# Kernel optimization log

Hardware: AMD Instinct MI355X
Metric: run time of the kernel (lower is better)

Reference implementation:

```python
import jax, jax.numpy as jnp
import numpy as np

V, P, H, NH, D, L, FF, W, NCLS = 50265, 4098, 768, 12, 64, 12, 3072, 256, 43

def _ln(x, g, b):
    m = jnp.mean(x, -1, keepdims=True)
    v = jnp.mean((x - m) ** 2, -1, keepdims=True)
    return (x - m) * jax.lax.rsqrt(v + 1e-5) * g + b

def _sliding_attn(h, mask, wq, bq, wk, bk, wv, bv):
    # Longformer sliding-window attention, one-sided window W=256 (total 513).
    B, S, _ = h.shape
    C = S // W  # number of query chunks
    split = lambda x: x.reshape(B, S, NH, D).transpose(0, 2, 1, 3)  # [B,NH,S,D]
    q = split(h @ wq + bq) * (1.0 / np.sqrt(D))
    k = split(h @ wk + bk)
    v = split(h @ wv + bv)
    # keys/values needed by query chunk c span absolute positions [c*W - W, c*W + 2W)
    idx = jnp.arange(3 * W)[None, :] + W * jnp.arange(C)[:, None]  # [C,3W] into padded seq
    kb = jnp.pad(k, ((0, 0), (0, 0), (W, W), (0, 0)))[:, :, idx]  # [B,NH,C,3W,D]
    vb = jnp.pad(v, ((0, 0), (0, 0), (W, W), (0, 0)))[:, :, idx]
    qc = q.reshape(B, NH, C, W, D)
    s = jnp.einsum('bhcqd,bhckd->bhcqk', qc, kb)  # [B,NH,C,W,3W]
    r = jnp.arange(W)[:, None]
    t = jnp.arange(3 * W)[None, :]
    band = (t - r >= 0) & (t - r <= 2 * W)  # |key_pos - query_pos| <= W
    km = jnp.pad(mask, ((0, 0), (W, W)))[:, idx] > 0  # [B,C,3W] valid (non-pad) keys
    m = band[None, None, None] & km[:, None, :, None, :]  # [B,1,C,W,3W]
    p = jax.nn.softmax(jnp.where(m, s, -1e9), axis=-1)
    o = jnp.einsum('bhcqk,bhckd->bhcqd', p, vb).reshape(B, NH, S, D)
    return o.transpose(0, 2, 1, 3).reshape(B, S, NH * D)

def _forward(input_ids, attention_mask, word_emb, pos_emb, tok_emb, emb_ln_g, emb_ln_b,
             Wq, bq, Wk, bk, Wv, bv, Wo, bo, ln1_g, ln1_b, Wi, bi, Wo2, bo2, ln2_g, ln2_b,
             cls_w1, cls_b1, cls_w2, cls_b2):
    B, S = input_ids.shape
    pos = jnp.arange(S) + 2  # RoBERTa-style offset (padding_idx=1)
    h = word_emb[input_ids] + pos_emb[pos][None] + tok_emb[0][None, None]
    h = _ln(h, emb_ln_g, emb_ln_b)
    mask = attention_mask
    def block(h, p):
        wq, bq_, wk, bk_, wv, bv_, wo, bo_, g1, b1, wi, bi_, wo2, bo2_, g2, b2 = p
        a = _sliding_attn(h, mask, wq, bq_, wk, bk_, wv, bv_)
        h = _ln(h + a @ wo + bo_, g1, b1)
        f = jax.nn.gelu(h @ wi + bi_, approximate=False)
        h = _ln(h + f @ wo2 + bo2_, g2, b2)
        return h, None
    h, _ = jax.lax.scan(block, h, (Wq, bq, Wk, bk, Wv, bv, Wo, bo, ln1_g, ln1_b,
                                   Wi, bi, Wo2, bo2, ln2_g, ln2_b))
    pooled = h[:, 0]  # CLS token
    x = jax.nn.relu(pooled @ cls_w1 + cls_b1)
    return x @ cls_w2 + cls_b2

def setup_inputs() -> dict:
    key = jax.random.key(0)
    ks = iter(jax.random.split(key, 64))
    def rn(shape):
        return jax.random.normal(next(ks), shape, dtype=jnp.float32) * 0.02
    return {
        'input_ids': jax.random.randint(next(ks), (2, 4096), 0, V, dtype=jnp.int32),
        'attention_mask': jnp.ones((2, 4096), dtype=jnp.int32),
        'word_emb': rn((V, H)), 'pos_emb': rn((P, H)), 'tok_emb': rn((1, H)),
        'emb_ln_g': jnp.ones(H), 'emb_ln_b': jnp.zeros(H),
        'Wq': rn((L, H, H)), 'bq': jnp.zeros((L, H)),
        'Wk': rn((L, H, H)), 'bk': jnp.zeros((L, H)),
        'Wv': rn((L, H, H)), 'bv': jnp.zeros((L, H)),
        'Wo': rn((L, H, H)), 'bo': jnp.zeros((L, H)),
        'ln1_g': jnp.ones((L, H)), 'ln1_b': jnp.zeros((L, H)),
        'Wi': rn((L, H, FF)), 'bi': jnp.zeros((L, FF)),
        'Wo2': rn((L, FF, H)), 'bo2': jnp.zeros((L, H)),
        'ln2_g': jnp.ones((L, H)), 'ln2_b': jnp.zeros((L, H)),
        'cls_w1': rn((H, 512)), 'cls_b1': jnp.zeros(512),
        'cls_w2': rn((512, NCLS)), 'cls_b2': jnp.zeros(NCLS),
    }

def reference(input_ids, attention_mask, word_emb, pos_emb, tok_emb, emb_ln_g, emb_ln_b,
              Wq, bq, Wk, bk, Wv, bv, Wo, bo, ln1_g, ln1_b, Wi, bi, Wo2, bo2, ln2_g, ln2_b,
              cls_w1, cls_b1, cls_w2, cls_b2):
    return _forward(input_ids, attention_mask, word_emb, pos_emb, tok_emb, emb_ln_g, emb_ln_b,
                    Wq, bq, Wk, bk, Wv, bv, Wo, bo, ln1_g, ln1_b, Wi, bi, Wo2, bo2, ln2_g, ln2_b,
                    cls_w1, cls_b1, cls_w2, cls_b2)
```

## Files before the change

### kernel.cpp

```cpp
#include <hip/hip_runtime.h>
#include <hip/hip_bf16.h>

typedef unsigned short u16;
typedef __attribute__((ext_vector_type(8))) short short8;
typedef __attribute__((ext_vector_type(4))) float f32x4;

__device__ __forceinline__ float bf2f(u16 x){
    union { unsigned u; float f; } c; c.u = ((unsigned)x) << 16; return c.f;
}
__device__ __forceinline__ u16 f2bf(float f){
    union { float f; unsigned u; } c; c.f = f;
    unsigned u = c.u;
    return (u16)((u + 0x7FFFu + ((u >> 16) & 1u)) >> 16);
}
__device__ __forceinline__ f32x4 MFMA(short8 a, short8 b, f32x4 c){
    return __builtin_amdgcn_mfma_f32_16x16x32_bf16(a, b, c, 0, 0, 0);
}
__device__ __forceinline__ void gld_lds16(const u16* g, u16* l){
    __builtin_amdgcn_global_load_lds((const __attribute__((address_space(1))) unsigned int*)g,
                                     (__attribute__((address_space(3))) unsigned int*)l, 16, 0, 0);
}

#define SEQ 4096
#define HID 768
#define QKVW 2304

template<int OUT_MODE, int ACT_GELU>
__global__ __launch_bounds__(256)
void gemm_bt(const u16* __restrict__ A, const u16* __restrict__ Bt,
             const float* __restrict__ bias, void* __restrict__ outp,
             int M, int N, int K, int Kc)
{
    __shared__ __align__(16) u16 As[3][128*32];
    __shared__ __align__(16) u16 Bs[3][128*32];
    const int tid  = threadIdx.x;
    const int w    = tid >> 6, lane = tid & 63;
    const int quad = lane >> 4, l16 = lane & 15;
    const int m0 = blockIdx.x * 128, n0 = blockIdx.y * 128;
    const int wm = (w >> 1) * 64, wn = (w & 1) * 64;
    const int kz0 = blockIdx.z * Kc;

    f32x4 acc[4][4];
    for (int i = 0; i < 4; i++) for (int j = 0; j < 4; j++)
        acc[i][j] = (f32x4){0.f, 0.f, 0.f, 0.f};

    const int c0 = tid, c1 = tid + 256;
    const int la0 = (w*64)*8;
    const int la1 = ((w+4)*64)*8;
    const u16* gA0 = A  + (size_t)(m0 + (c0>>2)) * K + (c0&3)*8 + kz0;
    const u16* gA1 = A  + (size_t)(m0 + (c1>>2)) * K + (c1&3)*8 + kz0;
    const u16* gB0 = Bt + (size_t)(n0 + (c0>>2)) * K + (c0&3)*8 + kz0;
    const u16* gB1 = Bt + (size_t)(n0 + (c1>>2)) * K + (c1&3)*8 + kz0;

    auto stage = [&](int buf, int k0) {
        gld_lds16(gA0 + k0, &As[buf][la0]);
        gld_lds16(gA1 + k0, &As[buf][la1]);
        gld_lds16(gB0 + k0, &Bs[buf][la0]);
        gld_lds16(gB1 + k0, &Bs[buf][la1]);
    };

    const int nk = Kc >> 5;
    stage(0, 0);
    stage(1, 32);
    for (int t = 0; t < nk; ++t) {
        if (t + 1 < nk) { asm volatile("s_waitcnt vmcnt(4)" ::: "memory"); }
        else            { asm volatile("s_waitcnt vmcnt(0)" ::: "memory"); }
        __builtin_amdgcn_s_barrier();
        if (t + 2 < nk) stage((t + 2) % 3, (t + 2) * 32);
        const int cur = t % 3;
        short8 af[4], bfr[4];
        for (int mt = 0; mt < 4; mt++)
            af[mt]  = *(const short8*)&As[cur][(wm + mt*16 + l16)*32 + quad*8];
        for (int nt = 0; nt < 4; nt++)
            bfr[nt] = *(const short8*)&Bs[cur][(wn + nt*16 + l16)*32 + quad*8];
        __builtin_amdgcn_s_setprio(1);
        for (int mt = 0; mt < 4; mt++)
            for (int nt = 0; nt < 4; nt++)
                acc[mt][nt] = MFMA(af[mt], bfr[nt], acc[mt][nt]);
        __builtin_amdgcn_s_setprio(0);
    }

    if (OUT_MODE == 0) {
        u16* out = (u16*)outp;
        for (int mt = 0; mt < 4; mt++) {
            const int rbase = m0 + wm + mt*16 + quad*4;
            for (int nt = 0; nt < 4; nt++) {
                const int col = n0 + wn + nt*16 + l16;
                const float bc = bias ? bias[col] : 0.f;
                f32x4 v = acc[mt][nt];
                for (int reg = 0; reg < 4; reg++) {
                    const size_t idx = (size_t)(rbase + reg) * N + col;
                    float x = v[reg] + bc;
                    if (ACT_GELU) x = 0.5f * x * (1.f + erff(x * 0.7071067811865476f));
                    out[idx] = f2bf(x);
                }
            }
        }
    } else {
        float* out = (float*)outp + (size_t)blockIdx.z * M * N;
        for (int mt = 0; mt < 4; mt++) {
            const int rbase = m0 + wm + mt*16 + quad*4;
            for (int nt = 0; nt < 4; nt++) {
                const int col = n0 + wn + nt*16 + l16;
                f32x4 v = acc[mt][nt];
                for (int reg = 0; reg < 4; reg++)
                    out[(size_t)(rbase + reg) * N + col] = v[reg];
            }
        }
    }
}

__global__ __launch_bounds__(256)
void prep_layer(const float* __restrict__ Wq, const float* __restrict__ Wk,
                const float* __restrict__ Wv, const float* __restrict__ Wo,
                const float* __restrict__ Wi, const float* __restrict__ Wo2,
                const float* __restrict__ bq, const float* __restrict__ bk,
                const float* __restrict__ bv,
                u16* __restrict__ WtQKV, u16* __restrict__ WtO,
                u16* __restrict__ WtI, u16* __restrict__ WtO2,
                float* __restrict__ bqkv)
{
    const int id  = blockIdx.x;
    const int tid = threadIdx.x;
    if (id == 6912) {
        for (int i = tid; i < QKVW; i += 256) {
            if (i < 768)       bqkv[i] = bq[i] * 0.125f;
            else if (i < 1536) bqkv[i] = bk[i - 768];
            else               bqkv[i] = bv[i - 1536];
        }
        return;
    }
    const float* src; u16* dst; int K, N, t; float scale = 1.f;
    if (id < 2304) {
        const int m = id / 576; t = id % 576; K = 768; N = 768;
        if      (m == 0) { src = Wq; dst = WtQKV;             scale = 0.125f; }
        else if (m == 1) { src = Wk; dst = WtQKV + 768*768; }
        else if (m == 2) { src = Wv; dst = WtQKV + 2*768*768; }
        else             { src = Wo; dst = WtO; }
    } else if (id < 4608) { t = id - 2304; K = 768;  N = 3072; src = Wi;  dst = WtI;  }
    else                  { t = id - 4608; K = 3072; N = 768;  src = Wo2; dst = WtO2; }

    const int ntx = N / 32;
    const int bx = (t / ntx) * 32, by = (t % ntx) * 32;
    __shared__ float tt[32][33];
    const int tx = tid & 31, ty = tid >> 5;
    for (int i = 0; i < 4; i++)
        tt[ty + i*8][tx] = src[(size_t)(bx + ty + i*8) * N + by + tx];
    __syncthreads();
    for (int i = 0; i < 4; i++)
        dst[(size_t)(by + ty + i*8) * K + bx + tx] = f2bf(tt[tx][ty + i*8] * scale);
}

__global__ void embed_kernel(const int* __restrict__ ids, const float* __restrict__ we,
                             const float* __restrict__ pe, const float* __restrict__ te,
                             u16* __restrict__ pb)
{
    const int t = blockIdx.x;
    const int s = t & (SEQ - 1);
    const int id = ids[t];
    const size_t wb = (size_t)id * HID;
    const size_t pbase = (size_t)(s + 2) * HID;
    for (int d = threadIdx.x; d < HID; d += 256)
        pb[(size_t)t * HID + d] = f2bf(we[wb + d] + pe[pbase + d] + te[d]);
}

__global__ __launch_bounds__(256)
void ln_kernel(const u16* __restrict__ pre, const float* __restrict__ resid,
               const float* __restrict__ g, const float* __restrict__ bta,
               float* __restrict__ h, u16* __restrict__ hb)
{
    const int t = blockIdx.x;
    float v[3], s = 0.f, s2 = 0.f;
    for (int i = 0; i < 3; i++) {
        const int d = threadIdx.x + i*256;
        float x = bf2f(pre[(size_t)t*HID + d]);
        if (resid) x += resid[(size_t)t*HID + d];
        v[i] = x; s += x; s2 += x*x;
    }
    for (int o = 32; o > 0; o >>= 1) { s += __shfl_xor(s, o, 64); s2 += __shfl_xor(s2, o, 64); }
    __shared__ float red[8];
    const int w = threadIdx.x >> 6, lane = threadIdx.x & 63;
    if (lane == 0) { red[w] = s; red[w+4] = s2; }
    __syncthreads();
    s  = red[0] + red[1] + red[2] + red[3];
    s2 = red[4] + red[5] + red[6] + red[7];
    const float mean = s * (1.f/768.f);
    const float var  = s2 * (1.f/768.f) - mean*mean;
    const float rs   = rsqrtf(fmaxf(var, 0.f) + 1e-5f);
    for (int i = 0; i < 3; i++) {
        const int d = threadIdx.x + i*256;
        const float y = (v[i] - mean) * rs * g[d] + bta[d];
        h [(size_t)t*HID + d] = y;
        hb[(size_t)t*HID + d] = f2bf(y);
    }
}

__global__ __launch_bounds__(256)
void ln_kernel_f32(const float* __restrict__ p0, const float* __restrict__ p1,
                   const float* __restrict__ bias, const float* __restrict__ resid,
                   const float* __restrict__ g, const float* __restrict__ bta,
                   float* __restrict__ h, u16* __restrict__ hb)
{
    const int t = blockIdx.x;
    float v[3], s = 0.f, s2 = 0.f;
    for (int i = 0; i < 3; i++) {
        const int d = threadIdx.x + i*256;
        const size_t ix = (size_t)t*HID + d;
        float x = p0[ix] + p1[ix] + bias[d] + resid[ix];
        v[i] = x; s += x; s2 += x*x;
    }
    for (int o = 32; o > 0; o >>= 1) { s += __shfl_xor(s, o, 64); s2 += __shfl_xor(s2, o, 64); }
    __shared__ float red[8];
    const int w = threadIdx.x >> 6, lane = threadIdx.x & 63;
    if (lane == 0) { red[w] = s; red[w+4] = s2; }
    __syncthreads();
    s  = red[0] + red[1] + red[2] + red[3];
    s2 = red[4] + red[5] + red[6] + red[7];
    const float mean = s * (1.f/768.f);
    const float var  = s2 * (1.f/768.f) - mean*mean;
    const float rs   = rsqrtf(fmaxf(var, 0.f) + 1e-5f);
    for (int i = 0; i < 3; i++) {
        const int d = threadIdx.x + i*256;
        const float y = (v[i] - mean) * rs * g[d] + bta[d];
        h [(size_t)t*HID + d] = y;
        hb[(size_t)t*HID + d] = f2bf(y);
    }
}

__global__ __launch_bounds__(256)
void attn_kernel(const u16* __restrict__ qkv, const int* __restrict__ amask,
                 u16* __restrict__ aout)
{
    const int bid = blockIdx.x;
    const int c  = bid & 15;
    const int hh = (bid >> 4) % 12;
    const int b  = bid / 192;
    const int tid = threadIdx.x;
    const int w = tid >> 6, lane = tid & 63;
    const int quad = lane >> 4, l16 = lane & 15;

    __shared__ __align__(16) u16 Vt[64 * 72];
    __shared__ __align__(16) u16 P[4 * 64 * 72];
    __shared__ int kmS[64];

    const u16* qbase = qkv + (size_t)(b * SEQ) * QKVW + hh * 64;

    short8 qa[4][2];
    const int qrow_base = c * 256 + w * 64;
    for (int mt = 0; mt < 4; mt++)
        for (int ks = 0; ks < 2; ks++) {
            const int t_q = qrow_base + mt*16 + l16;
            qa[mt][ks] = *(const short8*)(qbase + (size_t)t_q * QKVW + ks*32 + quad*8);
        }

    f32x4 oacc[4][5];
    for (int i = 0; i < 4; i++) for (int j = 0; j < 5; j++)
        oacc[i][j] = (f32x4){0.f, 0.f, 0.f, 0.f};
    short8 ones8;
    for (int j = 0; j < 8; j++) ones8[j] = 0x3F80;

    const int kglob0 = (c - 1) * 256;
    u16* Pw = P + w * (64 * 72);

    for (int ch = 0; ch < 12; ch++) {
        __syncthreads();
        {
            const int kl = tid & 63;
            const int dpart = tid >> 6;
            const int gk = kglob0 + ch*64 + kl;
            const bool gok = (gk >= 0 && gk < SEQ);
            for (int i = 0; i < 2; i++) {
                const int d0 = dpart*16 + i*8;
                short8 vv = {0,0,0,0,0,0,0,0};
                if (gok) vv = *(const short8*)(qkv + (size_t)(b*SEQ + gk)*QKVW + 1536 + hh*64 + d0);
                for (int j = 0; j < 8; j++) Vt[(d0 + j)*72 + kl] = (u16)vv[j];
            }
            if (tid < 64) kmS[kl] = gok ? amask[b*SEQ + gk] : 0;
        }
        __syncthreads();

        for (int nt = 0; nt < 4; nt++) {
            short8 kb0 = {0,0,0,0,0,0,0,0}, kb1 = {0,0,0,0,0,0,0,0};
            const int gk = kglob0 + ch*64 + nt*16 + l16;
            if (gk >= 0 && gk < SEQ) {
                const u16* kp = qkv + (size_t)(b*SEQ + gk)*QKVW + 768 + hh*64;
                kb0 = *(const short8*)(kp + quad*8);
                kb1 = *(const short8*)(kp + 32 + quad*8);
            }
            f32x4 sacc[4];
            for (int mt = 0; mt < 4; mt++) {
                sacc[mt] = (f32x4){0.f, 0.f, 0.f, 0.f};
                sacc[mt] = MFMA(qa[mt][0], kb0, sacc[mt]);
                sacc[mt] = MFMA(qa[mt][1], kb1, sacc[mt]);
            }
            const int tband = ch*64 + nt*16 + l16;
            const int km = kmS[nt*16 + l16];
            for (int mt = 0; mt < 4; mt++)
                for (int reg = 0; reg < 4; reg++) {
                    const int rloc = mt*16 + quad*4 + reg;
                    const int rq = w*64 + rloc;
                    const int dt = tband - rq;
                    float p = 0.f;
                    if (dt >= 0 && dt <= 512 && km) p = __expf(fminf(sacc[mt][reg], 30.f));
                    Pw[rloc*72 + nt*16 + l16] = f2bf(p);
                }
        }

        for (int ks = 0; ks < 2; ks++) {
            short8 vb[4];
            for (int nd = 0; nd < 4; nd++)
                vb[nd] = *(const short8*)&Vt[(nd*16 + l16)*72 + ks*32 + quad*8];
            for (int mt = 0; mt < 4; mt++) {
                short8 pa = *(const short8*)&Pw[(mt*16 + l16)*72 + ks*32 + quad*8];
                for (int nd = 0; nd < 4; nd++)
                    oacc[mt][nd] = MFMA(pa, vb[nd], oacc[mt][nd]);
                oacc[mt][4] = MFMA(pa, ones8, oacc[mt][4]);
            }
        }
    }

    u16* obase = aout + (size_t)(b * SEQ) * HID + hh * 64;
    for (int mt = 0; mt < 4; mt++)
        for (int reg = 0; reg < 4; reg++) {
            const int t_q = qrow_base + mt*16 + quad*4 + reg;
            const float l = oacc[mt][4][reg];
            const float rl = (l > 1e-30f) ? 1.f / l : 0.f;
            for (int nd = 0; nd < 4; nd++)
                obase[(size_t)t_q * HID + nd*16 + l16] = f2bf(oacc[mt][nd][reg] * rl);
        }
}

__global__ void cls1(const float* __restrict__ h, const float* __restrict__ w1,
                     const float* __restrict__ b1, float* __restrict__ x)
{
    const int j = blockIdx.x, b = blockIdx.y;
    const float* p = h + (size_t)(b * SEQ) * HID;
    float s = 0.f;
    for (int d = threadIdx.x; d < HID; d += 64) s += p[d] * w1[(size_t)d*512 + j];
    for (int o = 32; o > 0; o >>= 1) s += __shfl_xor(s, o, 64);
    if (threadIdx.x == 0) x[b*512 + j] = fmaxf(s + b1[j], 0.f);
}

__global__ void cls2(const float* __restrict__ x, const float* __restrict__ w2,
                     const float* __restrict__ b2, float* __restrict__ out)
{
    const int j = blockIdx.x, b = blockIdx.y;
    float s = 0.f;
    for (int d = threadIdx.x; d < 512; d += 64) s += x[b*512 + d] * w2[(size_t)d*43 + j];
    for (int o = 32; o > 0; o >>= 1) s += __shfl_xor(s, o, 64);
    if (threadIdx.x == 0) out[b*43 + j] = s + b2[j];
}

extern "C" void kernel_launch(void* const* d_in, const int* in_sizes, int n_in,
                              void* d_out, int out_size, void* d_ws, size_t ws_size,
                              hipStream_t stream)
{
    const int*   ids   = (const int*)d_in[0];
    const int*   amask = (const int*)d_in[1];
    const float* we  = (const float*)d_in[2];
    const float* pe  = (const float*)d_in[3];
    const float* te  = (const float*)d_in[4];
    const float* eg  = (const float*)d_in[5];
    const float* ebp = (const float*)d_in[6];
    const float* Wq_  = (const float*)d_in[7];
    const float* bq_  = (const float*)d_in[8];
    const float* Wk_  = (const float*)d_in[9];
    const float* bk_  = (const float*)d_in[10];
    const float* Wv_  = (const float*)d_in[11];
    const float* bv_  = (const float*)d_in[12];
    const float* Wo_  = (const float*)d_in[13];
    const float* bo_  = (const float*)d_in[14];
    const float* g1_  = (const float*)d_in[15];
    const float* b1_  = (const float*)d_in[16];
    const float* Wi_  = (const float*)d_in[17];
    const float* bi_  = (const float*)d_in[18];
    const float* Wo2_ = (const float*)d_in[19];
    const float* bo2_ = (const float*)d_in[20];
    const float* g2_  = (const float*)d_in[21];
    const float* b2_  = (const float*)d_in[22];
    const float* cw1  = (const float*)d_in[23];
    const float* cb1  = (const float*)d_in[24];
    const float* cw2  = (const float*)d_in[25];
    const float* cb2  = (const float*)d_in[26];

    char* wsb = (char*)d_ws;
    size_t off = 0;
    auto alloc = [&](size_t bytes) -> void* {
        void* p = wsb + off; off += (bytes + 255) & ~(size_t)255; return p;
    };
    const size_t MN = (size_t)8192 * 768;
    float* h    = (float*)alloc(MN*4);
    u16*   hb   = (u16*)  alloc(MN*2);
    u16*   pb   = (u16*)  alloc(MN*2);
    float* pf   = (float*)alloc(MN*4*2);
    u16*   U    = (u16*)  alloc((size_t)8192*3072*2);
    u16*   qkv  = U;
    u16*   ao   = U + (size_t)8192*QKVW;
    u16*   fbuf = U;
    u16*   WtQKV= (u16*)  alloc((size_t)QKVW*768*2);
    float* bqkv = (float*)alloc((size_t)QKVW*4);
    u16*   WtO  = (u16*)  alloc((size_t)768*768*2);
    u16*   WtI  = (u16*)  alloc((size_t)3072*768*2);
    u16*   WtO2 = (u16*)  alloc((size_t)768*3072*2);
    float* clsx = (float*)alloc((size_t)2*512*4);

    embed_kernel<<<8192, 256, 0, stream>>>(ids, we, pe, te, pb);
    ln_kernel<<<8192, 256, 0, stream>>>(pb, nullptr, eg, ebp, h, hb);

    for (int l = 0; l < 12; l++) {
        const size_t wHH = (size_t)l * 768 * 768;
        const size_t wHF = (size_t)l * 768 * 3072;
        prep_layer<<<6913, 256, 0, stream>>>(Wq_ + wHH, Wk_ + wHH, Wv_ + wHH, Wo_ + wHH,
                                             Wi_ + wHF, Wo2_ + wHF,
                                             bq_ + l*768, bk_ + l*768, bv_ + l*768,
                                             WtQKV, WtO, WtI, WtO2, bqkv);

        gemm_bt<0,0><<<dim3(64,18,1), 256, 0, stream>>>(hb, WtQKV, bqkv, qkv, 8192, QKVW, 768, 768);
        attn_kernel<<<384, 256, 0, stream>>>(qkv, amask, ao);
        gemm_bt<1,0><<<dim3(64,6,2), 256, 0, stream>>>(ao, WtO, nullptr, pf, 8192, 768, 768, 384);
        ln_kernel_f32<<<8192, 256, 0, stream>>>(pf, pf + MN, bo_ + l*768, h,
                                                g1_ + l*768, b1_ + l*768, h, hb);
        gemm_bt<0,1><<<dim3(64,24,1), 256, 0, stream>>>(hb, WtI, bi_ + l*3072, fbuf, 8192, 3072, 768, 768);
        gemm_bt<1,0><<<dim3(64,6,2), 256, 0, stream>>>(fbuf, WtO2, nullptr, pf, 8192, 768, 3072, 1536);
        ln_kernel_f32<<<8192, 256, 0, stream>>>(pf, pf + MN, bo2_ + l*768, h,
                                                g2_ + l*768, b2_ + l*768, h, hb);
    }

    cls1<<<dim3(512,2), 64, 0, stream>>>(h, cw1, cb1, clsx);
    cls2<<<dim3(43,2),  64, 0, stream>>>(clsx, cw2, cb2, (float*)d_out);
}
```

Before: 4.384 ms.

## Swizzle GEMM LDS tiles, remap blocks across XCDs, coalesce epilogue stores

Applies an XOR swizzle to the k-chunk placement in LDS, both on the async global-to-LDS loads and on the fragment reads, so the 16-byte MFMA operand reads avoid bank conflicts. Remaps the linear block id so that the 8 blocks sharing an XCD work on neighbouring M tiles of the same N column, improving L2 reuse of B. The bf16 epilogue now stages the output tile in padded LDS and writes it back as coalesced 16-byte row stores instead of scattered 2-byte stores. The remap hard-codes a grid shape of 64 M tiles per N column, which is only valid for particular M and N.

```diff
diff --git a/kernel.cpp b/kernel.cpp
--- a/kernel.cpp
+++ b/kernel.cpp
@@ -31,12 +31,16 @@
              const float* __restrict__ bias, void* __restrict__ outp,
              int M, int N, int K, int Kc)
 {
-    __shared__ __align__(16) u16 As[3][128*32];
-    __shared__ __align__(16) u16 Bs[3][128*32];
+    __shared__ __align__(16) u16 SM[6*4096];
     const int tid  = threadIdx.x;
     const int w    = tid >> 6, lane = tid & 63;
     const int quad = lane >> 4, l16 = lane & 15;
-    const int m0 = blockIdx.x * 128, n0 = blockIdx.y * 128;
+
+    const int bid = blockIdx.x + (gridDim.x * blockIdx.y);
+    const int xcd = bid & 7, idx = bid >> 3;
+    const int m0 = (xcd * 8 + (idx & 7)) * 128;
+    const int n0 = (idx >> 3) * 128;
+
     const int wm = (w >> 1) * 64, wn = (w & 1) * 64;
     const int kz0 = blockIdx.z * Kc;
 
@@ -45,19 +49,23 @@
         acc[i][j] = (f32x4){0.f, 0.f, 0.f, 0.f};
 
     const int c0 = tid, c1 = tid + 256;
+    const int r0 = c0 >> 2, kp0 = (c0 & 3) ^ ((r0 >> 1) & 3);
+    const int r1 = c1 >> 2, kp1 = (c1 & 3) ^ ((r1 >> 1) & 3);
     const int la0 = (w*64)*8;
     const int la1 = ((w+4)*64)*8;
-    const u16* gA0 = A  + (size_t)(m0 + (c0>>2)) * K + (c0&3)*8 + kz0;
-    const u16* gA1 = A  + (size_t)(m0 + (c1>>2)) * K + (c1&3)*8 + kz0;
-    const u16* gB0 = Bt + (size_t)(n0 + (c0>>2)) * K + (c0&3)*8 + kz0;
-    const u16* gB1 = Bt + (size_t)(n0 + (c1>>2)) * K + (c1&3)*8 + kz0;
+    const u16* gA0 = A  + (size_t)(m0 + r0) * K + kp0*8 + kz0;
+    const u16* gA1 = A  + (size_t)(m0 + r1) * K + kp1*8 + kz0;
+    const u16* gB0 = Bt + (size_t)(n0 + r0) * K + kp0*8 + kz0;
+    const u16* gB1 = Bt + (size_t)(n0 + r1) * K + kp1*8 + kz0;
 
     auto stage = [&](int buf, int k0) {
-        gld_lds16(gA0 + k0, &As[buf][la0]);
-        gld_lds16(gA1 + k0, &As[buf][la1]);
-        gld_lds16(gB0 + k0, &Bs[buf][la0]);
-        gld_lds16(gB1 + k0, &Bs[buf][la1]);
+        gld_lds16(gA0 + k0, SM + buf*4096 + la0);
+        gld_lds16(gA1 + k0, SM + buf*4096 + la1);
+        gld_lds16(gB0 + k0, SM + 12288 + buf*4096 + la0);
+        gld_lds16(gB1 + k0, SM + 12288 + buf*4096 + la1);
     };
+
+    const int sOff = (quad ^ ((l16 >> 1) & 3)) * 8;
 
     const int nk = Kc >> 5;
     stage(0, 0);
@@ -68,11 +76,13 @@
         __builtin_amdgcn_s_barrier();
         if (t + 2 < nk) stage((t + 2) % 3, (t + 2) * 32);
         const int cur = t % 3;
+        const u16* Ab = SM + cur*4096;
+        const u16* Bb = SM + 12288 + cur*4096;
         short8 af[4], bfr[4];
         for (int mt = 0; mt < 4; mt++)
-            af[mt]  = *(const short8*)&As[cur][(wm + mt*16 + l16)*32 + quad*8];
+            af[mt]  = *(const short8*)&Ab[(wm + mt*16 + l16)*32 + sOff];
         for (int nt = 0; nt < 4; nt++)
-            bfr[nt] = *(const short8*)&Bs[cur][(wn + nt*16 + l16)*32 + quad*8];
+            bfr[nt] = *(const short8*)&Bb[(wn + nt*16 + l16)*32 + sOff];
         __builtin_amdgcn_s_setprio(1);
         for (int mt = 0; mt < 4; mt++)
             for (int nt = 0; nt < 4; nt++)
@@ -82,19 +92,28 @@
 
     if (OUT_MODE == 0) {
         u16* out = (u16*)outp;
+        __syncthreads();
+        u16* Cs = SM;
+        const int CS = 132;
         for (int mt = 0; mt < 4; mt++) {
-            const int rbase = m0 + wm + mt*16 + quad*4;
+            const int rb = wm + mt*16 + quad*4;
             for (int nt = 0; nt < 4; nt++) {
-                const int col = n0 + wn + nt*16 + l16;
-                const float bc = bias ? bias[col] : 0.f;
+                const int cl = wn + nt*16 + l16;
+                const float bc = bias ? bias[n0 + cl] : 0.f;
                 f32x4 v = acc[mt][nt];
                 for (int reg = 0; reg < 4; reg++) {
-                    const size_t idx = (size_t)(rbase + reg) * N + col;
                     float x = v[reg] + bc;
                     if (ACT_GELU) x = 0.5f * x * (1.f + erff(x * 0.7071067811865476f));
-                    out[idx] = f2bf(x);
+                    Cs[(rb + reg)*CS + cl] = f2bf(x);
                 }
             }
+        }
+        __syncthreads();
+        for (int i = 0; i < 8; i++) {
+            const int slot = tid + i*256;
+            const int row = slot >> 4, seg = slot & 15;
+            short8 val = *(const short8*)&Cs[row*CS + seg*8];
+            *(short8*)&out[(size_t)(m0 + row) * N + n0 + seg*8] = val;
         }
     } else {
         float* out = (float*)outp + (size_t)blockIdx.z * M * N;
```

Result: faster. 3.939 ms (-10.1%).
